# Kernel tuning notes

Hardware: AMD Instinct MI355X
Metric: run time of the kernel (lower is better)

## Reference

```python
import jax, jax.numpy as jnp
import numpy as np

MASS = 2.8
DT = 0.016
RADIUS = 0.09
_angles = np.deg2rad(np.array([60.0, 130.0, 230.0, 300.0], dtype=np.float32))
# force_matrix rows: [-sin(a), cos(a), radius]  -> shape [3,4]
FORCE_MATRIX = jnp.asarray(np.stack([-np.sin(_angles), np.cos(_angles),
                                     np.full(4, RADIUS, dtype=np.float32)]).astype(np.float32))
# ik_matrix = stack([-sin, cos, radius]).T == FORCE_MATRIX.T  -> shape [4,3]
IK_MATRIX = FORCE_MATRIX.T


def setup_inputs() -> dict:
    key = jax.random.key(0)
    k1, k2 = jax.random.split(key)
    B, T = 8192, 1024
    return {
        "initial_state": jax.random.normal(k1, (B, 6), dtype=jnp.float32),
        "command_sequence": jax.random.normal(k2, (B, T, 3), dtype=jnp.float32),
        "com_offset": jnp.array([-0.05, 0.0], dtype=jnp.float32),
        "inertia_param": jnp.asarray(0.011, dtype=jnp.float32),
        "motor_gain_param": jnp.asarray(25.0, dtype=jnp.float32),
        "tire_grip_param": jnp.asarray(15.0, dtype=jnp.float32),
        "drag_viscous_param": jnp.array([1.0, 5.0, 1.0], dtype=jnp.float32),
        "drag_coulomb_param": jnp.array([0.5, 3.0, 0.5], dtype=jnp.float32),
    }


def _dynamics_step(state, cmd, com_offset, inertia, motor_gain, tire_grip, drag_v, drag_c):
    # state: [B,6] = [x, y, theta, vx_world, vy_world, omega]; cmd: [B,3]
    x, y, theta = state[:, 0], state[:, 1], state[:, 2]
    vx, vy, om = state[:, 3], state[:, 4], state[:, 5]
    c, s = jnp.cos(theta), jnp.sin(theta)
    vx_b = vx * c + vy * s
    vy_b = -vx * s + vy * c
    body_vel = jnp.stack([vx_b, vy_b, om], axis=1)            # [B,3]
    target_w = cmd @ IK_MATRIX.T                               # [B,4]
    curr_w = body_vel @ IK_MATRIX.T                            # [B,4]
    motor_force = motor_gain * (target_w - curr_w)
    F_geo = motor_force @ FORCE_MATRIX.T                       # [B,3]
    F_geo = (F_geo - tire_grip * (body_vel - cmd)
             - drag_v * body_vel - drag_c * jnp.sign(body_vel))
    Fx, Fy, Tau = F_geo[:, 0], F_geo[:, 1], F_geo[:, 2]
    dx, dy = com_offset[0], com_offset[1]
    Tau_com = Tau - (dx * Fy - dy * Fx)
    acc_x = Fx / MASS
    acc_y = Fy / MASS
    acc_al = Tau_com / inertia
    om2 = om * om
    ax_b = acc_x - acc_al * dy - om2 * dx
    ay_b = acc_y + acc_al * dx - om2 * dy
    ax_w = ax_b * c - ay_b * s
    ay_w = ax_b * s + ay_b * c
    nvx = vx + ax_w * DT
    nvy = vy + ay_w * DT
    nom = om + acc_al * DT
    nx = x + nvx * DT
    ny = y + nvy * DT
    nth = theta + nom * DT
    nth = jnp.arctan2(jnp.sin(nth), jnp.cos(nth))
    return jnp.stack([nx, ny, nth, nvx, nvy, nom], axis=1)


def reference(initial_state, command_sequence, com_offset, inertia_param,
              motor_gain_param, tire_grip_param, drag_viscous_param, drag_coulomb_param):
    inertia = jax.nn.softplus(inertia_param) + 0.0001
    motor_gain = jax.nn.softplus(motor_gain_param)
    tire_grip = jax.nn.softplus(tire_grip_param)
    drag_v = jax.nn.softplus(drag_viscous_param)
    drag_c = jax.nn.softplus(drag_coulomb_param)

    def step(state, cmd):
        nxt = _dynamics_step(state, cmd, com_offset, inertia,
                             motor_gain, tire_grip, drag_v, drag_c)
        return nxt, nxt

    cmds_t = jnp.transpose(command_sequence, (1, 0, 2))  # [T,B,3]
    _, states = jax.lax.scan(step, initial_state, cmds_t)  # [T,B,6]
    all_states = jnp.concatenate([initial_state[None], states], axis=0)  # [T+1,B,6]
    return jnp.transpose(all_states, (1, 0, 2))  # [B,T+1,6]
```

## Files before the change

### kernel.cpp

```cpp
#include <hip/hip_runtime.h>
#include <math.h>


#define MASS_F 2.8f
#define DT_F 0.016f

#define M00_F 2.6736481776669306f
#define M11_F 1.3263518223330697f
#define M12_F (-0.025701769743577074f)
#define M22_F 0.0324f

#define PI_F 3.14159265358979323846f
#define TWO_PI_F 6.28318530717958647692f

#define CHUNK 16

__device__ __forceinline__ float softplus_f(float x) {
    float ax = fabsf(x);
    return fmaxf(x, 0.0f) + log1pf(expf(-ax));
}

__device__ __forceinline__ float sgn_f(float v) {
    return (v > 0.0f ? 1.0f : 0.0f) - (v < 0.0f ? 1.0f : 0.0f);
}

__device__ __forceinline__ void fast_sincos(float th, float* sp, float* cp) {
    const float INV_PIO2 = 0.63661977236758134f;
    const float PIO2_HI  = 1.57079637050628662109375f;
    const float PIO2_LO  = -4.37113900018624283e-8f;
    float kf = rintf(th * INV_PIO2);
    int   k  = (int)kf;
    float r  = fmaf(-kf, PIO2_HI, th);
    r        = fmaf(-kf, PIO2_LO, r);
    float r2 = r * r;
    float ps = fmaf(r2, 2.7183114e-6f, -1.9515296e-4f);
    ps = fmaf(r2, ps, 8.3333310e-3f);
    ps = fmaf(r2, ps, -1.6666667e-1f);
    float sr = fmaf(r * r2, ps, r);
    float pc = fmaf(r2, 2.4760495e-5f, -1.3888889e-3f);
    pc = fmaf(r2, pc, 4.1666668e-2f);
    pc = fmaf(r2, pc, -0.5f);
    float cr = fmaf(r2, pc, 1.0f);
    int n = k & 3;
    float s = (n == 0) ? sr : (n == 1) ? cr : (n == 2) ? -sr : -cr;
    float c = (n == 0) ? cr : (n == 1) ? -sr : (n == 2) ? -cr : sr;
    *sp = s;
    *cp = c;
}

struct Coef {
    float A00, A11, A12, A22;
    float dv0, dv1, dv2;
    float dc0, dc1, dc2;
    float dx, dy, inv_mass, inv_inertia;
};

__device__ __forceinline__ void step_chunk(const float4 (&cb)[12], float* __restrict__ op,
                                           float& x, float& y, float& th,
                                           float& cth, float& sth,
                                           float& vxb, float& vyb, float& om,
                                           const Coef& K)
{
    float u[3 * CHUNK];
    #pragma unroll
    for (int i = 0; i < 12; ++i) {
        u[4 * i + 0] = cb[i].x;
        u[4 * i + 1] = cb[i].y;
        u[4 * i + 2] = cb[i].z;
        u[4 * i + 3] = cb[i].w;
    }

    #pragma unroll
    for (int j = 0; j < CHUNK; ++j) {
        const float u0 = u[3 * j + 0];
        const float u1 = u[3 * j + 1];
        const float u2 = u[3 * j + 2];

        const float ex = u0 - vxb;
        const float ey = u1 - vyb;
        const float ez = u2 - om;

        const float Fx = K.A00 * ex               - K.dv0 * vxb - K.dc0 * sgn_f(vxb);
        const float Fy = K.A11 * ey + K.A12 * ez  - K.dv1 * vyb - K.dc1 * sgn_f(vyb);
        const float Tz = K.A12 * ey + K.A22 * ez  - K.dv2 * om  - K.dc2 * sgn_f(om);

        const float Tc = Tz - (K.dx * Fy - K.dy * Fx);
        const float al = Tc * K.inv_inertia;
        const float om2 = om * om;

        const float axb = Fx * K.inv_mass - al * K.dy - om2 * K.dx;
        const float ayb = Fy * K.inv_mass + al * K.dx - om2 * K.dy;

        const float nom = om + al * DT_F;
        const float wx  = vxb + axb * DT_F;
        const float wy  = vyb + ayb * DT_F;

        const float dth = nom * DT_F;
        const float d2  = dth * dth;
        float sp = fmaf(d2, 8.3333333e-3f, -1.6666667e-1f);
        sp = fmaf(d2, sp, 1.0f);
        const float sd = dth * sp;
        float cp = fmaf(d2, 4.1666667e-2f, -0.5f);
        const float cd = fmaf(d2, cp, 1.0f);

        const float nvxb = fmaf(cd, wx,  sd * wy);
        const float nvyb = fmaf(cd, wy, -sd * wx);

        const float nvx = fmaf(cth, wx, -sth * wy);
        const float nvy = fmaf(sth, wx,  cth * wy);

        float nc = fmaf(cth, cd, -sth * sd);
        float ns = fmaf(sth, cd,  cth * sd);
        const float rn = fmaf(-0.5f, fmaf(nc, nc, ns * ns), 1.5f);
        nc *= rn;
        ns *= rn;

        x = fmaf(nvx, DT_F, x);
        y = fmaf(nvy, DT_F, y);
        float nth = th + dth;
        nth = (nth >  PI_F) ? nth - TWO_PI_F : nth;
        nth = (nth < -PI_F) ? nth + TWO_PI_F : nth;

        vxb = nvxb; vyb = nvyb; om = nom; th = nth; cth = nc; sth = ns;

        float* ot = op + 6 * j;
        ((float2*)ot)[0] = make_float2(x, y);
        ((float2*)ot)[1] = make_float2(nth, nvx);
        ((float2*)ot)[2] = make_float2(nvy, nom);
    }
}

__global__ __launch_bounds__(64, 1)
void omni_robot_kernel(const float* __restrict__ init_state,
                       const float* __restrict__ cmd_all,
                       const float* __restrict__ com_offset,
                       const float* __restrict__ inertia_p,
                       const float* __restrict__ gain_p,
                       const float* __restrict__ grip_p,
                       const float* __restrict__ drag_v_p,
                       const float* __restrict__ drag_c_p,
                       float* __restrict__ out,
                       int B, int T)
{
    const int b = blockIdx.x * blockDim.x + threadIdx.x;
    if (b >= B) return;

    const float inertia = softplus_f(inertia_p[0]) + 1e-4f;
    const float gain    = softplus_f(gain_p[0]);
    const float grip    = softplus_f(grip_p[0]);

    Coef K;
    K.A00 = gain * M00_F + grip;
    K.A11 = gain * M11_F + grip;
    K.A12 = gain * M12_F;
    K.A22 = gain * M22_F + grip;
    K.dv0 = softplus_f(drag_v_p[0]);
    K.dv1 = softplus_f(drag_v_p[1]);
    K.dv2 = softplus_f(drag_v_p[2]);
    K.dc0 = softplus_f(drag_c_p[0]);
    K.dc1 = softplus_f(drag_c_p[1]);
    K.dc2 = softplus_f(drag_c_p[2]);
    K.dx  = com_offset[0];
    K.dy  = com_offset[1];
    K.inv_mass    = 1.0f / MASS_F;
    K.inv_inertia = 1.0f / inertia;

    const float* st = init_state + (size_t)b * 6;
    float x  = st[0];
    float y  = st[1];
    float th = st[2];
    float vx = st[3];
    float vy = st[4];
    float om = st[5];

    const float* __restrict__ cmd = cmd_all + (size_t)b * T * 3;
    float* __restrict__ o = out + (size_t)b * (size_t)(T + 1) * 6;

    ((float2*)o)[0] = make_float2(x, y);
    ((float2*)o)[1] = make_float2(th, vx);
    ((float2*)o)[2] = make_float2(vy, om);

    float cth, sth;
    fast_sincos(th, &sth, &cth);
    float vxb = fmaf(vx, cth, vy * sth);
    float vyb = fmaf(vy, cth, -vx * sth);

    const float4* __restrict__ cmd4 = reinterpret_cast<const float4*>(cmd);
    const int nch = T / CHUNK;
    float* op = o + 6;

    if (nch > 0) {
        float4 bufA[12], bufB[12];
        #pragma unroll
        for (int i = 0; i < 12; ++i) bufA[i] = cmd4[i];

        for (int ch = 0; ch < nch; ch += 2) {
            {
                int pf = ch + 1; if (pf > nch - 1) pf = nch - 1;
                const float4* __restrict__ src = cmd4 + (size_t)pf * 12;
                #pragma unroll
                for (int i = 0; i < 12; ++i) bufB[i] = src[i];
            }
            step_chunk(bufA, op, x, y, th, cth, sth, vxb, vyb, om, K);
            op += 6 * CHUNK;

            {
                int pf = ch + 2; if (pf > nch - 1) pf = nch - 1;
                const float4* __restrict__ src = cmd4 + (size_t)pf * 12;
                #pragma unroll
                for (int i = 0; i < 12; ++i) bufA[i] = src[i];
            }
            if (ch + 1 < nch) {
                step_chunk(bufB, op, x, y, th, cth, sth, vxb, vyb, om, K);
                op += 6 * CHUNK;
            }
        }
    }

    if (nch * CHUNK < T) {
        vx = fmaf(cth, vxb, -sth * vyb);
        vy = fmaf(sth, vxb,  cth * vyb);
        for (int t = nch * CHUNK; t < T; ++t) {
            const float u0 = cmd[3 * t + 0];
            const float u1 = cmd[3 * t + 1];
            const float u2 = cmd[3 * t + 2];
            float c, s;
            fast_sincos(th, &s, &c);
            const float vxb_t = vx * c + vy * s;
            const float vyb_t = vy * c - vx * s;
            const float ex = u0 - vxb_t;
            const float ey = u1 - vyb_t;
            const float ez = u2 - om;
            const float Fx = K.A00 * ex               - K.dv0 * vxb_t - K.dc0 * sgn_f(vxb_t);
            const float Fy = K.A11 * ey + K.A12 * ez  - K.dv1 * vyb_t - K.dc1 * sgn_f(vyb_t);
            const float Tz = K.A12 * ey + K.A22 * ez  - K.dv2 * om    - K.dc2 * sgn_f(om);
            const float Tc = Tz - (K.dx * Fy - K.dy * Fx);
            const float al = Tc * K.inv_inertia;
            const float om2 = om * om;
            const float axb = Fx * K.inv_mass - al * K.dy - om2 * K.dx;
            const float ayb = Fy * K.inv_mass + al * K.dx - om2 * K.dy;
            const float axw = axb * c - ayb * s;
            const float ayw = axb * s + ayb * c;
            vx = vx + axw * DT_F;
            vy = vy + ayw * DT_F;
            om = om + al * DT_F;
            x  = x + vx * DT_F;
            y  = y + vy * DT_F;
            th = th + om * DT_F;
            th = (th >  PI_F) ? th - TWO_PI_F : th;
            th = (th < -PI_F) ? th + TWO_PI_F : th;
            float* ot = o + (size_t)(t + 1) * 6;
            ((float2*)ot)[0] = make_float2(x, y);
            ((float2*)ot)[1] = make_float2(th, vx);
            ((float2*)ot)[2] = make_float2(vy, om);
        }
    }
}

extern "C" void kernel_launch(void* const* d_in, const int* in_sizes, int n_in,
                              void* d_out, int out_size, void* d_ws, size_t ws_size,
                              hipStream_t stream) {
    const float* init_state = (const float*)d_in[0];
    const float* cmd        = (const float*)d_in[1];
    const float* com_offset = (const float*)d_in[2];
    const float* inertia_p  = (const float*)d_in[3];
    const float* gain_p     = (const float*)d_in[4];
    const float* grip_p     = (const float*)d_in[5];
    const float* drag_v_p   = (const float*)d_in[6];
    const float* drag_c_p   = (const float*)d_in[7];
    float* out = (float*)d_out;

    const int B = in_sizes[0] / 6;
    const int T = in_sizes[1] / (3 * B);

    const int block = 64;
    const int grid = (B + block - 1) / block;
    hipLaunchKernelGGL(omni_robot_kernel, dim3(grid), dim3(block), 0, stream,
                       init_state, cmd, com_offset, inertia_p, gain_p, grip_p,
                       drag_v_p, drag_c_p, out, B, T);
}
```

Measured before the change: 477.6 us.

## Stage command and output tiles through LDS for coalesced global access

Replaces per-thread strided row reads and writes with a cooperative transpose through shared memory. Lanes load command chunks for 16 rows at a time contiguously, stash them in padded LDS buffers, and each thread reads its own row from LDS; outputs are staged in LDS and written back two rows per wavefront instruction. Coefficients are also prescaled by inverse mass and inertia, and sign terms use copysign. It relies on the 64-thread block being a single wavefront, since no barriers are used, and it adds LDS traffic.

```diff
diff --git a/kernel.cpp b/kernel.cpp
--- a/kernel.cpp
+++ b/kernel.cpp
@@ -12,8 +12,11 @@
 
 #define PI_F 3.14159265358979323846f
 #define TWO_PI_F 6.28318530717958647692f
+#define INV_TWO_PI_F 0.15915494309189533577f
 
 #define CHUNK 16
+#define IN_STRIDE 49
+#define OUT_STRIDE 97
 
 __device__ __forceinline__ float softplus_f(float x) {
     float ax = fabsf(x);
@@ -49,84 +52,31 @@
 }
 
 struct Coef {
-    float A00, A11, A12, A22;
-    float dv0, dv1, dv2;
-    float dc0, dc1, dc2;
-    float dx, dy, inv_mass, inv_inertia;
+    float A00m, A11m, A12m, A22i, A12i;
+    float dv0m, dv1m, dv2i;
+    float dc0m, dc1m, dc2i;
+    float dxI, dyI;
+    float dx, dy;
 };
 
-__device__ __forceinline__ void step_chunk(const float4 (&cb)[12], float* __restrict__ op,
-                                           float& x, float& y, float& th,
-                                           float& cth, float& sth,
-                                           float& vxb, float& vyb, float& om,
-                                           const Coef& K)
-{
-    float u[3 * CHUNK];
+__device__ __forceinline__ void load_cmd_chunk(const float3* __restrict__ cmd3,
+                                               int B0, int B, int T, int ch,
+                                               int lane, float3 (&pf)[16]) {
+    const int rq = lane >> 4, m = lane & 15;
     #pragma unroll
-    for (int i = 0; i < 12; ++i) {
-        u[4 * i + 0] = cb[i].x;
-        u[4 * i + 1] = cb[i].y;
-        u[4 * i + 2] = cb[i].z;
-        u[4 * i + 3] = cb[i].w;
-    }
-
+    for (int i = 0; i < 16; ++i) {
+        int rg = B0 + 4 * i + rq;
+        if (rg >= B) rg = B - 1;
+        pf[i] = cmd3[(size_t)rg * T + (size_t)ch * CHUNK + m];
+    }
+}
+
+__device__ __forceinline__ void write_cmd_chunk(float* __restrict__ inrow,
+                                                int lane, const float3 (&pf)[16]) {
+    const int rq = lane >> 4, m = lane & 15;
     #pragma unroll
-    for (int j = 0; j < CHUNK; ++j) {
-        const float u0 = u[3 * j + 0];
-        const float u1 = u[3 * j + 1];
-        const float u2 = u[3 * j + 2];
-
-        const float ex = u0 - vxb;
-        const float ey = u1 - vyb;
-        const float ez = u2 - om;
-
-        const float Fx = K.A00 * ex               - K.dv0 * vxb - K.dc0 * sgn_f(vxb);
-        const float Fy = K.A11 * ey + K.A12 * ez  - K.dv1 * vyb - K.dc1 * sgn_f(vyb);
-        const float Tz = K.A12 * ey + K.A22 * ez  - K.dv2 * om  - K.dc2 * sgn_f(om);
-
-        const float Tc = Tz - (K.dx * Fy - K.dy * Fx);
-        const float al = Tc * K.inv_inertia;
-        const float om2 = om * om;
-
-        const float axb = Fx * K.inv_mass - al * K.dy - om2 * K.dx;
-        const float ayb = Fy * K.inv_mass + al * K.dx - om2 * K.dy;
-
-        const float nom = om + al * DT_F;
-        const float wx  = vxb + axb * DT_F;
-        const float wy  = vyb + ayb * DT_F;
-
-        const float dth = nom * DT_F;
-        const float d2  = dth * dth;
-        float sp = fmaf(d2, 8.3333333e-3f, -1.6666667e-1f);
-        sp = fmaf(d2, sp, 1.0f);
-        const float sd = dth * sp;
-        float cp = fmaf(d2, 4.1666667e-2f, -0.5f);
-        const float cd = fmaf(d2, cp, 1.0f);
-
-        const float nvxb = fmaf(cd, wx,  sd * wy);
-        const float nvyb = fmaf(cd, wy, -sd * wx);
-
-        const float nvx = fmaf(cth, wx, -sth * wy);
-        const float nvy = fmaf(sth, wx,  cth * wy);
-
-        float nc = fmaf(cth, cd, -sth * sd);
-        float ns = fmaf(sth, cd,  cth * sd);
-        const float rn = fmaf(-0.5f, fmaf(nc, nc, ns * ns), 1.5f);
-        nc *= rn;
-        ns *= rn;
-
-        x = fmaf(nvx, DT_F, x);
-        y = fmaf(nvy, DT_F, y);
-        float nth = th + dth;
-        nth = (nth >  PI_F) ? nth - TWO_PI_F : nth;
-        nth = (nth < -PI_F) ? nth + TWO_PI_F : nth;
-
-        vxb = nvxb; vyb = nvyb; om = nom; th = nth; cth = nc; sth = ns;
-
-        float* ot = op + 6 * j;
-        ((float2*)ot)[0] = make_float2(x, y);
-        ((float2*)ot)[1] = make_float2(nth, nvx);
-        ((float2*)ot)[2] = make_float2(nvy, nom);
+    for (int i = 0; i < 16; ++i) {
+        *reinterpret_cast<float3*>(&inrow[(4 * i + rq) * IN_STRIDE + 3 * m]) = pf[i];
     }
 }
 
@@ -142,30 +92,38 @@
                        float* __restrict__ out,
                        int B, int T)
 {
-    const int b = blockIdx.x * blockDim.x + threadIdx.x;
-    if (b >= B) return;
+    __shared__ float inbuf[2][64 * IN_STRIDE];
+    __shared__ float outbuf[64 * OUT_STRIDE];
+
+    const int lane = threadIdx.x;
+    const int B0   = blockIdx.x * 64;
+    const int b    = B0 + lane;
+    const int bc   = (b < B) ? b : (B - 1);
 
     const float inertia = softplus_f(inertia_p[0]) + 1e-4f;
     const float gain    = softplus_f(gain_p[0]);
     const float grip    = softplus_f(grip_p[0]);
+    const float inv_mass    = 1.0f / MASS_F;
+    const float inv_inertia = 1.0f / inertia;
 
     Coef K;
-    K.A00 = gain * M00_F + grip;
-    K.A11 = gain * M11_F + grip;
-    K.A12 = gain * M12_F;
-    K.A22 = gain * M22_F + grip;
-    K.dv0 = softplus_f(drag_v_p[0]);
-    K.dv1 = softplus_f(drag_v_p[1]);
-    K.dv2 = softplus_f(drag_v_p[2]);
-    K.dc0 = softplus_f(drag_c_p[0]);
-    K.dc1 = softplus_f(drag_c_p[1]);
-    K.dc2 = softplus_f(drag_c_p[2]);
-    K.dx  = com_offset[0];
-    K.dy  = com_offset[1];
-    K.inv_mass    = 1.0f / MASS_F;
-    K.inv_inertia = 1.0f / inertia;
-
-    const float* st = init_state + (size_t)b * 6;
+    K.A00m = (gain * M00_F + grip) * inv_mass;
+    K.A11m = (gain * M11_F + grip) * inv_mass;
+    K.A12m = (gain * M12_F) * inv_mass;
+    K.A12i = (gain * M12_F) * inv_inertia;
+    K.A22i = (gain * M22_F + grip) * inv_inertia;
+    K.dv0m = softplus_f(drag_v_p[0]) * inv_mass;
+    K.dv1m = softplus_f(drag_v_p[1]) * inv_mass;
+    K.dv2i = softplus_f(drag_v_p[2]) * inv_inertia;
+    K.dc0m = softplus_f(drag_c_p[0]) * inv_mass;
+    K.dc1m = softplus_f(drag_c_p[1]) * inv_mass;
+    K.dc2i = softplus_f(drag_c_p[2]) * inv_inertia;
+    K.dx   = com_offset[0];
+    K.dy   = com_offset[1];
+    K.dxI  = K.dx * MASS_F * inv_inertia;
+    K.dyI  = K.dy * MASS_F * inv_inertia;
+
+    const float* st = init_state + (size_t)bc * 6;
     float x  = st[0];
     float y  = st[1];
     float th = st[2];
@@ -173,51 +131,111 @@
     float vy = st[4];
     float om = st[5];
 
-    const float* __restrict__ cmd = cmd_all + (size_t)b * T * 3;
-    float* __restrict__ o = out + (size_t)b * (size_t)(T + 1) * 6;
-
-    ((float2*)o)[0] = make_float2(x, y);
-    ((float2*)o)[1] = make_float2(th, vx);
-    ((float2*)o)[2] = make_float2(vy, om);
+    float* __restrict__ o = out + (size_t)bc * (size_t)(T + 1) * 6;
+    if (b < B) {
+        ((float2*)o)[0] = make_float2(x, y);
+        ((float2*)o)[1] = make_float2(th, vx);
+        ((float2*)o)[2] = make_float2(vy, om);
+    }
 
     float cth, sth;
     fast_sincos(th, &sth, &cth);
     float vxb = fmaf(vx, cth, vy * sth);
     float vyb = fmaf(vy, cth, -vx * sth);
 
-    const float4* __restrict__ cmd4 = reinterpret_cast<const float4*>(cmd);
+    const float3* __restrict__ cmd3 = reinterpret_cast<const float3*>(cmd_all);
     const int nch = T / CHUNK;
-    float* op = o + 6;
 
     if (nch > 0) {
-        float4 bufA[12], bufB[12];
-        #pragma unroll
-        for (int i = 0; i < 12; ++i) bufA[i] = cmd4[i];
-
-        for (int ch = 0; ch < nch; ch += 2) {
+        float3 pf[16];
+        load_cmd_chunk(cmd3, B0, B, T, 0, lane, pf);
+        write_cmd_chunk(&inbuf[0][0], lane, pf);
+        int cur = 0;
+
+        for (int ch = 0; ch < nch; ++ch) {
+            const int pfch = (ch + 1 < nch) ? (ch + 1) : (nch - 1);
+            load_cmd_chunk(cmd3, B0, B, T, pfch, lane, pf);
+
+            const float* __restrict__ urow = &inbuf[cur][lane * IN_STRIDE];
+            float* __restrict__ orow = &outbuf[lane * OUT_STRIDE];
+            #pragma unroll
+            for (int j = 0; j < CHUNK; ++j) {
+                const float3 u = *reinterpret_cast<const float3*>(&urow[3 * j]);
+
+                const float ex = u.x - vxb;
+                const float ey = u.y - vyb;
+                const float ez = u.z - om;
+
+                const float Fx = fmaf(K.A00m, ex, -fmaf(K.dv0m, vxb, copysignf(K.dc0m, vxb)));
+                const float Fy = fmaf(K.A11m, ey, fmaf(K.A12m, ez, -fmaf(K.dv1m, vyb, copysignf(K.dc1m, vyb))));
+                const float Tz = fmaf(K.A12i, ey, fmaf(K.A22i, ez, -fmaf(K.dv2i, om, copysignf(K.dc2i, om))));
+
+                const float al  = fmaf(K.dyI, Fx, fmaf(-K.dxI, Fy, Tz));
+                const float om2 = om * om;
+
+                const float axb = fmaf(-al, K.dy, fmaf(-om2, K.dx, Fx));
+                const float ayb = fmaf( al, K.dx, fmaf(-om2, K.dy, Fy));
+
+                const float nom = fmaf(al, DT_F, om);
+                const float wx  = fmaf(axb, DT_F, vxb);
+                const float wy  = fmaf(ayb, DT_F, vyb);
+
+                const float dth = nom * DT_F;
+                const float d2  = dth * dth;
+                float sp = fmaf(d2, 8.3333333e-3f, -1.6666667e-1f);
+                sp = fmaf(d2, sp, 1.0f);
+                const float sd = dth * sp;
+                const float cp = fmaf(d2, 4.1666667e-2f, -0.5f);
+                const float cd = fmaf(d2, cp, 1.0f);
+
+                const float nvxb = fmaf(cd, wx,  sd * wy);
+                const float nvyb = fmaf(cd, wy, -sd * wx);
+
+                const float nvx = fmaf(cth, wx, -(sth * wy));
+                const float nvy = fmaf(sth, wx,  cth * wy);
+
+                float nc = fmaf(cth, cd, -(sth * sd));
+                float ns = fmaf(sth, cd,  cth * sd);
+                const float rn = fmaf(-0.5f, fmaf(nc, nc, ns * ns), 1.5f);
+                nc *= rn;
+                ns *= rn;
+
+                x = fmaf(nvx, DT_F, x);
+                y = fmaf(nvy, DT_F, y);
+                float nth = th + dth;
+                nth = fmaf(-rintf(nth * INV_TWO_PI_F), TWO_PI_F, nth);
+
+                vxb = nvxb; vyb = nvyb; om = nom; th = nth; cth = nc; sth = ns;
+
+                float* ot = orow + 6 * j;
+                ot[0] = x;   ot[1] = y;   ot[2] = nth;
+                ot[3] = nvx; ot[4] = nvy; ot[5] = nom;
+            }
+
+            write_cmd_chunk(&inbuf[cur ^ 1][0], lane, pf);
+
             {
-                int pf = ch + 1; if (pf > nch - 1) pf = nch - 1;
-                const float4* __restrict__ src = cmd4 + (size_t)pf * 12;
+                const int rh = lane >> 5, m2 = lane & 31;
+                const size_t tbase = (size_t)(ch * CHUNK + 1) * 6 + 3 * m2;
                 #pragma unroll
-                for (int i = 0; i < 12; ++i) bufB[i] = src[i];
+                for (int i = 0; i < 32; ++i) {
+                    const int r = 2 * i + rh;
+                    const float3 v = *reinterpret_cast<const float3*>(
+                        &outbuf[r * OUT_STRIDE + 3 * m2]);
+                    const int rg = B0 + r;
+                    if (rg < B) {
+                        *reinterpret_cast<float3*>(
+                            out + (size_t)rg * (size_t)(T + 1) * 6 + tbase) = v;
+                    }
+                }
             }
-            step_chunk(bufA, op, x, y, th, cth, sth, vxb, vyb, om, K);
-            op += 6 * CHUNK;
-
-            {
-                int pf = ch + 2; if (pf > nch - 1) pf = nch - 1;
-                const float4* __restrict__ src = cmd4 + (size_t)pf * 12;
-                #pragma unroll
-                for (int i = 0; i < 12; ++i) bufA[i] = src[i];
-            }
-            if (ch + 1 < nch) {
-                step_chunk(bufB, op, x, y, th, cth, sth, vxb, vyb, om, K);
-                op += 6 * CHUNK;
-            }
+
+            cur ^= 1;
         }
     }
 
-    if (nch * CHUNK < T) {
+    if (nch * CHUNK < T && b < B) {
+        const float* __restrict__ cmd = cmd_all + (size_t)b * T * 3;
         vx = fmaf(cth, vxb, -sth * vyb);
         vy = fmaf(sth, vxb,  cth * vyb);
         for (int t = nch * CHUNK; t < T; ++t) {
@@ -231,14 +249,13 @@
             const float ex = u0 - vxb_t;
             const float ey = u1 - vyb_t;
             const float ez = u2 - om;
-            const float Fx = K.A00 * ex               - K.dv0 * vxb_t - K.dc0 * sgn_f(vxb_t);
-            const float Fy = K.A11 * ey + K.A12 * ez  - K.dv1 * vyb_t - K.dc1 * sgn_f(vyb_t);
-            const float Tz = K.A12 * ey + K.A22 * ez  - K.dv2 * om    - K.dc2 * sgn_f(om);
-            const float Tc = Tz - (K.dx * Fy - K.dy * Fx);
-            const float al = Tc * K.inv_inertia;
+            const float Fx = fmaf(K.A00m, ex, -fmaf(K.dv0m, vxb_t, copysignf(K.dc0m, vxb_t)));
+            const float Fy = fmaf(K.A11m, ey, fmaf(K.A12m, ez, -fmaf(K.dv1m, vyb_t, copysignf(K.dc1m, vyb_t))));
+            const float Tz = fmaf(K.A12i, ey, fmaf(K.A22i, ez, -fmaf(K.dv2i, om, copysignf(K.dc2i, om))));
+            const float al  = fmaf(K.dyI, Fx, fmaf(-K.dxI, Fy, Tz));
             const float om2 = om * om;
-            const float axb = Fx * K.inv_mass - al * K.dy - om2 * K.dx;
-            const float ayb = Fy * K.inv_mass + al * K.dx - om2 * K.dy;
+            const float axb = fmaf(-al, K.dy, fmaf(-om2, K.dx, Fx));
+            const float ayb = fmaf( al, K.dx, fmaf(-om2, K.dy, Fy));
             const float axw = axb * c - ayb * s;
             const float ayw = axb * s + ayb * c;
             vx = vx + axw * DT_F;
@@ -247,8 +264,7 @@
             x  = x + vx * DT_F;
             y  = y + vy * DT_F;
             th = th + om * DT_F;
-            th = (th >  PI_F) ? th - TWO_PI_F : th;
-            th = (th < -PI_F) ? th + TWO_PI_F : th;
+            th = fmaf(-rintf(th * INV_TWO_PI_F), TWO_PI_F, th);
             float* ot = o + (size_t)(t + 1) * 6;
             ((float2*)ot)[0] = make_float2(x, y);
             ((float2*)ot)[1] = make_float2(th, vx);
```

Measured after the change: 513.3 us. 7.5% more time.
